# Kernel optimization log

Measured on AMD Instinct MI355X. Metric: run time of the kernel, lower is better.

## Reference

```python
import jax, jax.numpy as jnp
import numpy as np

KERNEL_SIZE = 25  # moving-average window (matches init kernel_size)


def setup_inputs() -> dict:
    key = jax.random.key(0)
    ks = jax.random.split(key, 5)
    B, T, N, D, O = 128, 336, 325, 3, 96
    return {
        "x": jax.random.normal(ks[0], (B, T, N, D), dtype=jnp.float32),
        "W_season": jax.random.normal(ks[1], (N, T, O), dtype=jnp.float32) * 0.02,
        "b_season": jax.random.normal(ks[2], (N, O), dtype=jnp.float32) * 0.02,
        "W_trend": jax.random.normal(ks[3], (N, T, O), dtype=jnp.float32) * 0.02,
        "b_trend": jax.random.normal(ks[4], (N, O), dtype=jnp.float32) * 0.02,
    }


def _moving_avg(z, k):
    # z: (M, T); replicate-pad (k-1)//2 at both ends, then mean over window k, stride 1.
    p = (k - 1) // 2
    xp = jnp.pad(z, ((0, 0), (p, p)), mode="edge")
    cs = jnp.concatenate(
        [jnp.zeros((z.shape[0], 1), z.dtype), jnp.cumsum(xp, axis=1)], axis=1
    )
    return (cs[:, k:] - cs[:, :-k]) / k  # (M, T) for odd k


def reference(x, W_season, b_season, W_trend, b_trend):
    B, T, N, D = x.shape
    O = W_season.shape[-1]
    # (B,T,N,D) -> (B,N,D,T) -> flat (B*N*D, T)
    z = x.transpose(0, 2, 3, 1).reshape(B * N * D, T)
    mean = _moving_avg(z, KERNEL_SIZE)
    res = z - mean
    BD = B * D
    # Faithful to the original slicing res[B*n*D : B*(n+1)*D]: contiguous blocks
    # of B*D rows per node -> reshape to (N, B*D, T).
    res_n = res.reshape(N, BD, T)
    mean_n = mean.reshape(N, BD, T)
    out_res = jnp.einsum("nbt,nto->nbo", res_n, W_season) + b_season[:, None, :]
    out_mean = jnp.einsum("nbt,nto->nbo", mean_n, W_trend) + b_trend[:, None, :]
    out = (out_res + out_mean).transpose(1, 0, 2)  # stack dim=1 -> (B*D, N, O)
    # torch .view(B, N, D, O) on contiguous (B*D, N, O), then permute(0,3,1,2)
    out = out.reshape(B, N, D, O).transpose(0, 3, 1, 2)  # (B, O, N, D)
    return out
```

## Files before the change

kernel.cpp:

```cpp
#include <hip/hip_runtime.h>
#include <hip/hip_bf16.h>

typedef __attribute__((ext_vector_type(8))) short short8;
typedef __attribute__((ext_vector_type(4))) float f32x4;
typedef unsigned short ushort_t;
typedef unsigned int uint32;

#define T_DIM   336
#define N_NODES 325
#define O_DIM   96
#define BD      384
#define ND      975
#define XB      327600
#define KT      96
#define NSTEP   4
#define MT      128
#define AST     104
#define BST     104
#define BSEG    10240
#define WTO     32256
#define WP_T    120

static __device__ __forceinline__ uint32 pk2bf(float a, float b) {
    union { __hip_bfloat16 h; ushort_t u; } x, y;
    x.h = __float2bfloat16(a); y.h = __float2bfloat16(b);
    return ((uint32)y.u << 16) | x.u;
}
static __device__ __forceinline__ ushort_t f2bf(float f) {
    union { __hip_bfloat16 h; ushort_t u; } cv;
    cv.h = __float2bfloat16(f);
    return cv.u;
}
static __device__ __forceinline__ float bf2f(ushort_t u) {
    union { ushort_t u; __hip_bfloat16 h; } cv;
    cv.u = u;
    return __bfloat162float(cv.h);
}

static __device__ __forceinline__ void gload_lds16(const void* g, void* l) {
    __builtin_amdgcn_global_load_lds(
        (const __attribute__((address_space(1))) void*)g,
        (__attribute__((address_space(3))) void*)l, 16, 0, 0);
}

__global__ __launch_bounds__(576, 7)
void dlinear_wprep(const float* __restrict__ Ws, const float* __restrict__ bs,
                   const float* __restrict__ Wt, const float* __restrict__ bt,
                   ushort_t* __restrict__ Bpack, float* __restrict__ biasArr)
{
    __shared__ ushort_t Wdl[WP_T][O_DIM];
    __shared__ ushort_t Bout[O_DIM * BST];

    const int nn  = blockIdx.x;
    const int s   = blockIdx.y;
    const int tid = threadIdx.x;
    const int t0  = s * KT;

    const float* wsn = Ws + (size_t)nn * WTO;
    const float* wtn = Wt + (size_t)nn * WTO;

    {
        const int o   = tid % O_DIM;
        const int tA  = tid / O_DIM;
        #pragma unroll
        for (int it = 0; it < 20; ++it) {
            int t  = tA + it * 6;
            int tg = t0 - 12 + t;
            float v = 0.f;
            if (tg >= 0 && tg < T_DIM) v = wtn[tg*O_DIM + o] - wsn[tg*O_DIM + o];
            Wdl[t][o] = f2bf(v);
        }
    }
    if (s == 0 && tid < O_DIM)
        biasArr[nn*O_DIM + tid] = bs[nn*O_DIM + tid] + bt[nn*O_DIM + tid];
    __syncthreads();

    const int kc = tid / O_DIM;
    const int o  = tid - kc*O_DIM;
    const int k0 = kc * 16;

    float wsv[16];
    #pragma unroll
    for (int j = 0; j < 16; ++j) {
        int vv = t0 + k0 + j;
        wsv[j] = (vv < T_DIM) ? wsn[vv*O_DIM + o] : 0.f;
    }

    float S = 0.f;
    #pragma unroll
    for (int j = 0; j < 25; ++j) S += bf2f(Wdl[k0 + j][o]);

    uint32* bo32 = (uint32*)(Bout + o * BST);
    float prev = 0.f;
    #pragma unroll
    for (int j = 0; j < 16; ++j) {
        const int k = k0 + j;
        const int v = t0 + k;
        float val = 0.f;
        if (v < T_DIM) {
            float V = S;
            if (v == 0) {
                V = 0.f;
                #pragma unroll
                for (int t = 0; t <= 12; ++t) V += (float)(13 - t) * bf2f(Wdl[12 + t][o]);
            } else if (v == T_DIM - 1) {
                V = 0.f;
                #pragma unroll
                for (int t = 0; t <= 12; ++t) V += (float)(t + 1) * bf2f(Wdl[47 + t][o]);
            }
            val = wsv[j] + V * (1.0f/25.0f);
        }
        if (j & 1) bo32[k >> 1] = pk2bf(prev, val); else prev = val;
        if (j < 15) S += bf2f(Wdl[k + 25][o]) - bf2f(Wdl[k][o]);
    }
    __syncthreads();

    {
        const uint32* src = (const uint32*)Bout;
        uint32* dst = (uint32*)(Bpack + (size_t)(nn*4 + s) * BSEG);
        for (int d = tid; d < (O_DIM*BST)/2; d += 576)
            dst[d] = src[d];
    }
}

__global__ __launch_bounds__(512, 6)
void dlinear_gemm(const float* __restrict__ x,
                  const ushort_t* __restrict__ Bpack,
                  const float* __restrict__ biasArr,
                  float* __restrict__ Cws)
{
    __shared__ ushort_t Btile[BSEG];
    __shared__ ushort_t Atile[MT][AST];

    const int tid = threadIdx.x;
    const int bid = blockIdx.x;
    const int nn  = bid / 3;
    const int m0  = (bid % 3) * MT;
    const int r_base = nn * BD + m0;

    const int m   = tid & (MT-1);
    const int tb  = (tid >> 7) * 24;
    const int r   = r_base + m;
    const int bI  = r / ND;
    const int rem = r - bI * ND;
    const float* xp = x + (size_t)bI * XB + rem;

    const ushort_t* bsrc = Bpack + (size_t)nn * (4*BSEG);

    const int wave = tid >> 6;
    const int lane = tid & 63;
    const int wm = wave & 3;
    const int wn = wave >> 2;
    const int a_row0 = wm*32 + (lane & 15);
    const int b_col0 = wn*48 + (lane & 15);
    const int ksub   = (lane >> 4) * 8;

    f32x4 acc[2][3];
    #pragma unroll
    for (int i = 0; i < 2; ++i)
        #pragma unroll
        for (int j = 0; j < 3; ++j)
            acc[i][j] = (f32x4){0.f, 0.f, 0.f, 0.f};

    for (int s = 0; s < NSTEP; ++s) {
        __syncthreads();

        {
            const ushort_t* bs_s = bsrc + (size_t)s * BSEG;
            gload_lds16(bs_s + (size_t)tid*8,        &Btile[tid*8]);
            gload_lds16(bs_s + (size_t)(tid+512)*8,  &Btile[(tid+512)*8]);
            if (tid < 256)
                gload_lds16(bs_s + (size_t)(tid+1024)*8, &Btile[(tid+1024)*8]);
        }

        const int t0 = s * KT;
        #pragma unroll
        for (int h = 0; h < 2; ++h) {
            float v[12];
            #pragma unroll
            for (int u = 0; u < 12; ++u) {
                int t  = t0 + tb + h*12 + u;
                int tc = t < T_DIM ? t : (T_DIM-1);
                v[u] = __builtin_nontemporal_load(&xp[tc * ND]);
            }
            uint32 p[6];
            #pragma unroll
            for (int u = 0; u < 6; ++u) p[u] = pk2bf(v[2*u], v[2*u+1]);
            uint32* arow = (uint32*)&Atile[m][tb + h*12];
            *(uint2*)&arow[0] = make_uint2(p[0], p[1]);
            *(uint2*)&arow[2] = make_uint2(p[2], p[3]);
            *(uint2*)&arow[4] = make_uint2(p[4], p[5]);
        }
        __syncthreads();

        #pragma unroll
        for (int kc = 0; kc < 3; ++kc) {
            const int k = kc*32 + ksub;
            short8 a0 = *(const short8*)&Atile[a_row0     ][k];
            short8 a1 = *(const short8*)&Atile[a_row0 + 16][k];
            short8 b0 = *(const short8*)&Btile[(b_col0     )*BST + k];
            short8 b1 = *(const short8*)&Btile[(b_col0 + 16)*BST + k];
            short8 b2 = *(const short8*)&Btile[(b_col0 + 32)*BST + k];
            acc[0][0] = __builtin_amdgcn_mfma_f32_16x16x32_bf16(a0, b0, acc[0][0], 0, 0, 0);
            acc[1][0] = __builtin_amdgcn_mfma_f32_16x16x32_bf16(a1, b0, acc[1][0], 0, 0, 0);
            acc[0][1] = __builtin_amdgcn_mfma_f32_16x16x32_bf16(a0, b1, acc[0][1], 0, 0, 0);
            acc[1][1] = __builtin_amdgcn_mfma_f32_16x16x32_bf16(a1, b1, acc[1][1], 0, 0, 0);
            acc[0][2] = __builtin_amdgcn_mfma_f32_16x16x32_bf16(a0, b2, acc[0][2], 0, 0, 0);
            acc[1][2] = __builtin_amdgcn_mfma_f32_16x16x32_bf16(a1, b2, acc[1][2], 0, 0, 0);
        }
    }

    float* Cbase = Cws + (size_t)r_base * O_DIM;
    const float* bfp = biasArr + nn * O_DIM;
    const int rsub = (lane >> 4) * 4;
    #pragma unroll
    for (int fm = 0; fm < 2; ++fm) {
        #pragma unroll
        for (int fn = 0; fn < 3; ++fn) {
            const int col = b_col0 + fn*16;
            const float bv = bfp[col];
            #pragma unroll
            for (int j = 0; j < 4; ++j) {
                const int rowm = wm*32 + fm*16 + rsub + j;
                Cbase[rowm*O_DIM + col] = acc[fm][fn][j] + bv;
            }
        }
    }
}

__global__ __launch_bounds__(256)
void dlinear_out(const float* __restrict__ Cws, float* __restrict__ out)
{
    __shared__ float tile[65][97];
    const int m   = blockIdx.x;
    const int nn0 = blockIdx.y * 65;
    const int tid = threadIdx.x;

    for (int idx = tid; idx < 65*O_DIM; idx += 256) {
        int nni = idx / O_DIM;
        int o   = idx - nni*O_DIM;
        tile[nni][o] = Cws[(size_t)((nn0 + nni)*BD + m)*O_DIM + o];
    }
    __syncthreads();
    const int b = m / 3;
    const int g = m - b*3;
    float* obase = out + (size_t)b*93600 + g*N_NODES + nn0;
    for (int idx = tid; idx < 65*O_DIM; idx += 256) {
        int o   = idx / 65;
        int nni = idx - o*65;
        obase[o*ND + nni] = tile[nni][o];
    }
}

extern "C" void kernel_launch(void* const* d_in, const int* in_sizes, int n_in,
                              void* d_out, int out_size, void* d_ws, size_t ws_size,
                              hipStream_t stream)
{
    const float* x  = (const float*)d_in[0];
    const float* Ws = (const float*)d_in[1];
    const float* bs = (const float*)d_in[2];
    const float* Wt = (const float*)d_in[3];
    const float* bt = (const float*)d_in[4];
    float* out = (float*)d_out;
    float* Cws = (float*)d_ws;

    ushort_t* Bpack  = (ushort_t*)d_out;
    float*    biasAr = (float*)d_out + 6656000;

    dlinear_wprep<<<dim3(N_NODES, 4), dim3(576), 0, stream>>>(Ws, bs, Wt, bt, Bpack, biasAr);
    dlinear_gemm <<<dim3(975),        dim3(512), 0, stream>>>(x, Bpack, biasAr, Cws);
    dlinear_out  <<<dim3(384, 5),     dim3(256), 0, stream>>>(Cws, out);
}
```

Measured before the change: 112.5 us.

## Prefetch all x loads upfront and double-buffer weight tiles in GEMM

The GEMM kernel now uses 96-row M tiles with 384 threads and 1300 blocks. Each thread issues all of its x loads for the four K steps at the start, holding them in registers. Weight tiles are double-buffered in LDS so the global-to-LDS copy of the next step overlaps with MFMA work. This targets global load latency stalls at each step, at the cost of about 96 extra live registers per thread and lower occupancy from the launch-bounds change (512,6 to 384,3).

Result: slower. 126.9 us (+12.8%).

```diff
diff --git a/kernel.cpp b/kernel.cpp
--- a/kernel.cpp
+++ b/kernel.cpp
@@ -14,10 +14,11 @@
 #define XB      327600
 #define KT      96
 #define NSTEP   4
-#define MT      128
+#define MT      96
 #define AST     104
 #define BST     104
 #define BSEG    10240
+#define BLDS    9984
 #define WTO     32256
 #define WP_T    120
 
@@ -123,23 +124,23 @@
     }
 }
 
-__global__ __launch_bounds__(512, 6)
+__global__ __launch_bounds__(384, 3)
 void dlinear_gemm(const float* __restrict__ x,
                   const ushort_t* __restrict__ Bpack,
                   const float* __restrict__ biasArr,
                   float* __restrict__ Cws)
 {
-    __shared__ ushort_t Btile[BSEG];
     __shared__ ushort_t Atile[MT][AST];
+    __shared__ ushort_t Btile[2][BLDS];
 
     const int tid = threadIdx.x;
     const int bid = blockIdx.x;
-    const int nn  = bid / 3;
-    const int m0  = (bid % 3) * MT;
-    const int r_base = nn * BD + m0;
-
-    const int m   = tid & (MT-1);
-    const int tb  = (tid >> 7) * 24;
+    const int nn  = bid >> 2;
+    const int mt  = bid & 3;
+    const int r_base = nn * BD + mt * MT;
+
+    const int m   = tid % MT;
+    const int tb  = (tid / MT) * 24;
     const int r   = r_base + m;
     const int bI  = r / ND;
     const int rem = r - bI * ND;
@@ -149,8 +150,8 @@
 
     const int wave = tid >> 6;
     const int lane = tid & 63;
-    const int wm = wave & 3;
-    const int wn = wave >> 2;
+    const int wm = wave % 3;
+    const int wn = wave / 3;
     const int a_row0 = wm*32 + (lane & 15);
     const int b_col0 = wn*48 + (lane & 15);
     const int ksub   = (lane >> 4) * 8;
@@ -162,45 +163,61 @@
         for (int j = 0; j < 3; ++j)
             acc[i][j] = (f32x4){0.f, 0.f, 0.f, 0.f};
 
+    {
+        #pragma unroll
+        for (int i = 0; i < 3; ++i)
+            gload_lds16(bsrc + (size_t)(tid + 384*i)*8, &Btile[0][(tid + 384*i)*8]);
+        if (tid < 96)
+            gload_lds16(bsrc + (size_t)(tid + 1152)*8, &Btile[0][(tid + 1152)*8]);
+        const ushort_t* b1 = bsrc + BSEG;
+        #pragma unroll
+        for (int i = 0; i < 3; ++i)
+            gload_lds16(b1 + (size_t)(tid + 384*i)*8, &Btile[1][(tid + 384*i)*8]);
+        if (tid < 96)
+            gload_lds16(b1 + (size_t)(tid + 1152)*8, &Btile[1][(tid + 1152)*8]);
+    }
+    float v0[24], v1[24], v2[24], v3[24];
+    #pragma unroll
+    for (int u = 0; u < 24; ++u)
+        v0[u] = __builtin_nontemporal_load(&xp[(tb + u) * ND]);
+    #pragma unroll
+    for (int u = 0; u < 24; ++u)
+        v1[u] = __builtin_nontemporal_load(&xp[(96 + tb + u) * ND]);
+    #pragma unroll
+    for (int u = 0; u < 24; ++u)
+        v2[u] = __builtin_nontemporal_load(&xp[(192 + tb + u) * ND]);
+    #pragma unroll
+    for (int u = 0; u < 24; ++u) {
+        int t  = 288 + tb + u;
+        int tc = t < T_DIM ? t : (T_DIM-1);
+        v3[u] = __builtin_nontemporal_load(&xp[tc * ND]);
+    }
+    __builtin_amdgcn_sched_barrier(0);
+
+#define PACK_A(VARR)                                                      \
+    {                                                                     \
+        uint32 p[12];                                                     \
+        _Pragma("unroll")                                                 \
+        for (int u = 0; u < 12; ++u) p[u] = pk2bf(VARR[2*u], VARR[2*u+1]);\
+        uint32* arow = (uint32*)&Atile[m][tb];                            \
+        *(uint4*)&arow[0] = make_uint4(p[0], p[1], p[2],  p[3]);          \
+        *(uint4*)&arow[4] = make_uint4(p[4], p[5], p[6],  p[7]);          \
+        *(uint4*)&arow[8] = make_uint4(p[8], p[9], p[10], p[11]);         \
+    }
+
+    PACK_A(v0);
+    __syncthreads();
+
+    #pragma unroll
     for (int s = 0; s < NSTEP; ++s) {
-        __syncthreads();
-
-        {
-            const ushort_t* bs_s = bsrc + (size_t)s * BSEG;
-            gload_lds16(bs_s + (size_t)tid*8,        &Btile[tid*8]);
-            gload_lds16(bs_s + (size_t)(tid+512)*8,  &Btile[(tid+512)*8]);
-            if (tid < 256)
-                gload_lds16(bs_s + (size_t)(tid+1024)*8, &Btile[(tid+1024)*8]);
-        }
-
-        const int t0 = s * KT;
-        #pragma unroll
-        for (int h = 0; h < 2; ++h) {
-            float v[12];
-            #pragma unroll
-            for (int u = 0; u < 12; ++u) {
-                int t  = t0 + tb + h*12 + u;
-                int tc = t < T_DIM ? t : (T_DIM-1);
-                v[u] = __builtin_nontemporal_load(&xp[tc * ND]);
-            }
-            uint32 p[6];
-            #pragma unroll
-            for (int u = 0; u < 6; ++u) p[u] = pk2bf(v[2*u], v[2*u+1]);
-            uint32* arow = (uint32*)&Atile[m][tb + h*12];
-            *(uint2*)&arow[0] = make_uint2(p[0], p[1]);
-            *(uint2*)&arow[2] = make_uint2(p[2], p[3]);
-            *(uint2*)&arow[4] = make_uint2(p[4], p[5]);
-        }
-        __syncthreads();
-
         #pragma unroll
         for (int kc = 0; kc < 3; ++kc) {
             const int k = kc*32 + ksub;
             short8 a0 = *(const short8*)&Atile[a_row0     ][k];
             short8 a1 = *(const short8*)&Atile[a_row0 + 16][k];
-            short8 b0 = *(const short8*)&Btile[(b_col0     )*BST + k];
-            short8 b1 = *(const short8*)&Btile[(b_col0 + 16)*BST + k];
-            short8 b2 = *(const short8*)&Btile[(b_col0 + 32)*BST + k];
+            short8 b0 = *(const short8*)&Btile[s & 1][(b_col0     )*BST + k];
+            short8 b1 = *(const short8*)&Btile[s & 1][(b_col0 + 16)*BST + k];
+            short8 b2 = *(const short8*)&Btile[s & 1][(b_col0 + 32)*BST + k];
             acc[0][0] = __builtin_amdgcn_mfma_f32_16x16x32_bf16(a0, b0, acc[0][0], 0, 0, 0);
             acc[1][0] = __builtin_amdgcn_mfma_f32_16x16x32_bf16(a1, b0, acc[1][0], 0, 0, 0);
             acc[0][1] = __builtin_amdgcn_mfma_f32_16x16x32_bf16(a0, b1, acc[0][1], 0, 0, 0);
@@ -208,7 +225,26 @@
             acc[0][2] = __builtin_amdgcn_mfma_f32_16x16x32_bf16(a0, b2, acc[0][2], 0, 0, 0);
             acc[1][2] = __builtin_amdgcn_mfma_f32_16x16x32_bf16(a1, b2, acc[1][2], 0, 0, 0);
         }
-    }
+
+        if (s < NSTEP - 1) {
+            __syncthreads();
+
+            if (s < 2) {
+                const ushort_t* bn = bsrc + (size_t)(s + 2) * BSEG;
+                ushort_t* bl = &Btile[s & 1][0];
+                #pragma unroll
+                for (int i = 0; i < 3; ++i)
+                    gload_lds16(bn + (size_t)(tid + 384*i)*8, bl + (tid + 384*i)*8);
+                if (tid < 96)
+                    gload_lds16(bn + (size_t)(tid + 1152)*8, bl + (tid + 1152)*8);
+            }
+            if (s == 0)      PACK_A(v1)
+            else if (s == 1) PACK_A(v2)
+            else             PACK_A(v3)
+            __syncthreads();
+        }
+    }
+#undef PACK_A
 
     float* Cbase = Cws + (size_t)r_base * O_DIM;
     const float* bfp = biasArr + nn * O_DIM;
@@ -268,6 +304,6 @@
     float*    biasAr = (float*)d_out + 6656000;
 
     dlinear_wprep<<<dim3(N_NODES, 4), dim3(576), 0, stream>>>(Ws, bs, Wt, bt, Bpack, biasAr);
-    dlinear_gemm <<<dim3(975),        dim3(512), 0, stream>>>(x, Bpack, biasAr, Cws);
+    dlinear_gemm <<<dim3(1300),       dim3(384), 0, stream>>>(x, Bpack, biasAr, Cws);
     dlinear_out  <<<dim3(384, 5),     dim3(256), 0, stream>>>(Cws, out);
 }
```
